# Performance work log

Hardware: AMD Instinct MI355X
Metric: run time of the kernel (lower is better)

The kernel has to match this reference:

```python
import jax, jax.numpy as jnp
import numpy as np

# Irrep layout of node_vec: 128x0e | 64x1e (64*3) | 32x2e (32*5)
MUL0, MUL1, MUL2 = 128, 64, 32
A = 32  # node_attr scalar channels (32x0e)
N = 8192


def setup_inputs() -> dict:
    key = jax.random.key(0)
    ks = jax.random.split(key, 12)
    f32 = jnp.float32
    return {
        "node_vec": jax.random.normal(ks[0], (N, MUL0 + 3 * MUL1 + 5 * MUL2), f32),
        "node_embedding": jax.random.normal(ks[1], (N, A), f32),
        # fctp_1: TP(input, attr) -> gated irreps (scalars + gates + vectors)
        "W1s": jax.random.normal(ks[2], (MUL0, A, MUL0), f32),          # 0e x 0e -> 0e
        "b1s": jnp.zeros((MUL0,), f32),
        "W1g": jax.random.normal(ks[3], (MUL0, A, MUL1 + MUL2), f32),   # 0e x 0e -> gate 0e
        "b1g": jnp.zeros((MUL1 + MUL2,), f32),
        "W1v1": jax.random.normal(ks[4], (MUL1, A, MUL1), f32),         # 1e x 0e -> 1e
        "W1v2": jax.random.normal(ks[5], (MUL2, A, MUL2), f32),         # 2e x 0e -> 2e
        # fctp_2: TP(mlp_mid, attr) -> 32x0e (only scalar path allowed by CG rules)
        "W2": jax.random.normal(ks[6], (MUL0, A, A), f32),
        "b2": jnp.zeros((A,), f32),
        # output network: LinearRS(32->32) + SiLU + LinearRS(32->1)
        "W3": jax.random.normal(ks[7], (A, A), f32),
        "b3": jnp.zeros((A,), f32),
        "W4": jax.random.normal(ks[8], (A, 1), f32),
        "b4": jnp.zeros((1,), f32),
    }


def reference(node_vec, node_embedding, W1s, b1s, W1g, b1g, W1v1, W1v2, W2, b2, W3, b3, W4, b4):
    n = node_vec.shape[0]
    attr = node_embedding
    # split features by irrep degree
    s = node_vec[:, :MUL0]                                         # [n,128]   0e
    v1 = node_vec[:, MUL0:MUL0 + 3 * MUL1].reshape(n, MUL1, 3)     # [n,64,3]  1e
    v2 = node_vec[:, MUL0 + 3 * MUL1:].reshape(n, MUL2, 5)         # [n,32,5]  2e

    inv = lambda u: 1.0 / np.sqrt(u * A).astype(np.float32)

    # ---- fctp_1: fully-connected TP with scalar attr (l x 0e -> l per-path mixing) ----
    s_mid = jnp.einsum('nu,nv,uvw->nw', s, attr, W1s) * inv(MUL0) + b1s
    g = jnp.einsum('nu,nv,uvw->nw', s, attr, W1g) * inv(MUL0) + b1g
    v1_mid = jnp.einsum('num,nv,uvw->nwm', v1, attr, W1v1) * inv(MUL1)
    v2_mid = jnp.einsum('num,nv,uvw->nwm', v2, attr, W1v2) * inv(MUL2)

    # ---- SwishGate: SiLU on scalars, sigmoid gates on vectors ----
    s_act = jax.nn.silu(s_mid)
    gate = jax.nn.sigmoid(g)
    v1_g = v1_mid * gate[:, :MUL1, None]
    v2_g = v2_mid * gate[:, MUL1:, None]
    # NOTE: v1_g/v2_g have no allowed CG path into the 0e output of fctp_2 (l x 0 -> 0
    # only for l=0), so they do not contribute — exactly as in the original module.
    del v1_g, v2_g

    # ---- fctp_2: mlp_mid x attr -> 32x0e (scalar path only) ----
    h = jnp.einsum('nu,nv,uvw->nw', s_act, attr, W2) * inv(MUL0) + b2

    # ---- output network: LinearRS + SiLU + LinearRS ----
    h = jax.nn.silu(h @ (W3 / np.sqrt(A).astype(np.float32)) + b3)
    pred_energy = h @ (W4 / np.sqrt(A).astype(np.float32)) + b4     # [n,1]
    return pred_energy
```

## Files before the change

kernel.cpp:

```cpp
#include <hip/hip_runtime.h>

typedef _Float16 f16;
typedef f16 f16x8 __attribute__((ext_vector_type(8)));
typedef f16 f16x4 __attribute__((ext_vector_type(4)));
typedef float f32x4 __attribute__((ext_vector_type(4)));

__global__ __launch_bounds__(256) void prep_kernel(
    const float* __restrict__ node_vec, const float* __restrict__ W1s,
    const float* __restrict__ W2, f16* __restrict__ s_bf,
    f16* __restrict__ W1G, f16* __restrict__ W2G)
{
    const int b = blockIdx.x, t = threadIdx.x;
    if (b < 512) {
        int j = b * 256 + t;
        int n = j >> 4, c8 = (j & 15) * 8;
        float4 a = *(const float4*)(node_vec + (size_t)n * 480 + c8);
        float4 c = *(const float4*)(node_vec + (size_t)n * 480 + c8 + 4);
        f16x8 o = { (f16)a.x, (f16)a.y, (f16)a.z, (f16)a.w,
                    (f16)c.x, (f16)c.y, (f16)c.z, (f16)c.w };
        *(f16x8*)(s_bf + (size_t)n * 128 + c8) = o;
    } else if (b < 1024) {
        int bb = b - 512;
        int cb = bb >> 2, u0 = (bb & 3) * 32;
        int v = t >> 3, u = u0 + (t & 7) * 4;
        f16x4 o = { (f16)W1s[(size_t)(u + 0) * 4096 + v * 128 + cb],
                    (f16)W1s[(size_t)(u + 1) * 4096 + v * 128 + cb],
                    (f16)W1s[(size_t)(u + 2) * 4096 + v * 128 + cb],
                    (f16)W1s[(size_t)(u + 3) * 4096 + v * 128 + cb] };
        *(f16x4*)(W1G + (size_t)(32 * cb + v) * 128 + u) = o;
    } else {
        int bb = b - 1024;
        int cb = bb >> 2, u0 = (bb & 3) * 32;
        int v = t >> 3, u = u0 + (t & 7) * 4;
        f16x4 o = { (f16)W2[(size_t)(u + 0) * 1024 + v * 32 + cb],
                    (f16)W2[(size_t)(u + 1) * 1024 + v * 32 + cb],
                    (f16)W2[(size_t)(u + 2) * 1024 + v * 32 + cb],
                    (f16)W2[(size_t)(u + 3) * 1024 + v * 32 + cb] };
        *(f16x4*)(W2G + (size_t)(32 * cb + v) * 128 + u) = o;
    }
}

template <int SILU>
__global__ __launch_bounds__(256, 2) void gemm_g(
    const f16* __restrict__ A, const f16* __restrict__ B,
    const float* __restrict__ attr, const float* __restrict__ bias,
    void* __restrict__ out)
{
    __shared__ __align__(16) unsigned char smem[69632];
    f16* A_lds = (f16*)smem;
    f16* B_lds = (f16*)smem + 128 * 136;

    const int t  = threadIdx.x;
    const int n0 = blockIdx.x * 128;
    const int c0 = blockIdx.y * 128;

    #pragma unroll
    for (int i = 0; i < 8; ++i) {
        int idx = t + 256 * i;
        int r = idx >> 4, c8 = (idx & 15) * 8;
        *(uint4*)(A_lds + r * 136 + c8) = *(const uint4*)(A + (size_t)(n0 + r) * 128 + c8);
        *(uint4*)(B_lds + r * 136 + c8) = *(const uint4*)(B + (size_t)(c0 + r) * 128 + c8);
    }
    __syncthreads();

    const int wv = t >> 6, l = t & 63, lr = l & 15, q = l >> 4;
    const int r0 = 32 * wv;

    f32x4 acc0[8], acc1[8];
    #pragma unroll
    for (int ct = 0; ct < 8; ++ct) { acc0[ct] = f32x4{0,0,0,0}; acc1[ct] = f32x4{0,0,0,0}; }

    #pragma unroll
    for (int ks = 0; ks < 4; ++ks) {
        f16x8 a0 = *(const f16x8*)(A_lds + (r0 + lr) * 136 + ks * 32 + q * 8);
        f16x8 a1 = *(const f16x8*)(A_lds + (r0 + 16 + lr) * 136 + ks * 32 + q * 8);
        #pragma unroll
        for (int ct = 0; ct < 8; ++ct) {
            f16x8 bf = *(const f16x8*)(B_lds + (16 * ct + lr) * 136 + ks * 32 + q * 8);
            acc0[ct] = __builtin_amdgcn_mfma_f32_16x16x32_f16(a0, bf, acc0[ct], 0, 0, 0);
            acc1[ct] = __builtin_amdgcn_mfma_f32_16x16x32_f16(a1, bf, acc1[ct], 0, 0, 0);
        }
    }

    float at[2][4][2];
    #pragma unroll
    for (int mt = 0; mt < 2; ++mt)
        #pragma unroll
        for (int reg = 0; reg < 4; ++reg) {
            int row = n0 + r0 + 16 * mt + q * 4 + reg;
            at[mt][reg][0] = attr[(size_t)row * 32 + lr];
            at[mt][reg][1] = attr[(size_t)row * 32 + 16 + lr];
        }

    #pragma unroll
    for (int mt = 0; mt < 2; ++mt)
        #pragma unroll
        for (int w = 0; w < 4; ++w) {
            f32x4 e0 = mt ? acc1[2 * w] : acc0[2 * w];
            f32x4 e1 = mt ? acc1[2 * w + 1] : acc0[2 * w + 1];
            float pv[4];
            #pragma unroll
            for (int reg = 0; reg < 4; ++reg)
                pv[reg] = e0[reg] * at[mt][reg][0] + e1[reg] * at[mt][reg][1];
            #pragma unroll
            for (int m = 1; m <= 8; m <<= 1) {
                #pragma unroll
                for (int reg = 0; reg < 4; ++reg)
                    pv[reg] += __shfl_xor(pv[reg], m);
            }
            if (lr == 0) {
                int wglob = (c0 >> 5) + w;
                float bv = bias[wglob];
                #pragma unroll
                for (int reg = 0; reg < 4; ++reg) {
                    int row = n0 + r0 + 16 * mt + q * 4 + reg;
                    float val = pv[reg] * 0.015625f + bv;
                    if (SILU) {
                        ((f16*)out)[(size_t)row * 128 + wglob] =
                            (f16)(val / (1.f + __expf(-val)));
                    } else {
                        ((float*)out)[(size_t)row * 32 + wglob] = val;
                    }
                }
            }
        }
}

__global__ __launch_bounds__(256) void head_kernel(
    const float* __restrict__ h, const float* __restrict__ W3,
    const float* __restrict__ b3, const float* __restrict__ W4,
    const float* __restrict__ b4, float* __restrict__ out)
{
    int tid = blockIdx.x * 256 + threadIdx.x;
    int n = tid >> 5, j = tid & 31;
    const float inv = 0.17677669529663687f;
    const float* hr = h + (size_t)n * 32;
    float acc = 0.f;
    #pragma unroll
    for (int i = 0; i < 32; ++i) acc += hr[i] * W3[i * 32 + j];
    float tv = acc * inv + b3[j];
    float g  = tv / (1.f + __expf(-tv));
    float p  = g * W4[j] * inv;
    #pragma unroll
    for (int m = 16; m >= 1; m >>= 1) p += __shfl_xor(p, m, 32);
    if (j == 0) out[n] = p + b4[0];
}

extern "C" void kernel_launch(void* const* d_in, const int* in_sizes, int n_in,
                              void* d_out, int out_size, void* d_ws, size_t ws_size,
                              hipStream_t stream)
{
    const float* node_vec = (const float*)d_in[0];
    const float* attr     = (const float*)d_in[1];
    const float* W1s      = (const float*)d_in[2];
    const float* b1s      = (const float*)d_in[3];
    const float* W2       = (const float*)d_in[8];
    const float* b2       = (const float*)d_in[9];
    const float* W3       = (const float*)d_in[10];
    const float* b3       = (const float*)d_in[11];
    const float* W4       = (const float*)d_in[12];
    const float* b4       = (const float*)d_in[13];
    float* out = (float*)d_out;

    char* ws = (char*)d_ws;
    f16*   s_bf  = (f16*)(ws);
    f16*   W1G   = (f16*)(ws + (2048u << 10));
    f16*   W2G   = (f16*)(ws + (3072u << 10));
    f16*   s_act = (f16*)(ws + (3328u << 10));
    float* h     = (float*)(ws + (5376u << 10));

    prep_kernel<<<1152, 256, 0, stream>>>(node_vec, W1s, W2, s_bf, W1G, W2G);
    gemm_g<1><<<dim3(64, 32), 256, 0, stream>>>(s_bf, W1G, attr, b1s, (void*)s_act);
    gemm_g<0><<<dim3(64, 8),  256, 0, stream>>>(s_act, W2G, attr, b2, (void*)h);
    head_kernel<<<1024, 256, 0, stream>>>(h, W3, b3, W4, b4, out);
}
```

Before: 131.6 us.

## Persist weight tile per block and loop over row subtiles with double-buffered A

```diff
diff --git a/kernel.cpp b/kernel.cpp
--- a/kernel.cpp
+++ b/kernel.cpp
@@ -40,90 +40,121 @@
     }
 }
 
-template <int SILU>
-__global__ __launch_bounds__(256, 2) void gemm_g(
+template <int NSUB, int SILU>
+__global__ __launch_bounds__(256, 1) void gemm_bs(
     const f16* __restrict__ A, const f16* __restrict__ B,
     const float* __restrict__ attr, const float* __restrict__ bias,
     void* __restrict__ out)
 {
-    __shared__ __align__(16) unsigned char smem[69632];
-    f16* A_lds = (f16*)smem;
-    f16* B_lds = (f16*)smem + 128 * 136;
+    __shared__ __align__(16) f16 B_lds[128 * 136];
+    __shared__ __align__(16) f16 A_lds[2][128 * 136];
 
     const int t  = threadIdx.x;
-    const int n0 = blockIdx.x * 128;
-    const int c0 = blockIdx.y * 128;
+    const int N0 = blockIdx.x * (NSUB * 128);
+    const int C0 = blockIdx.y * 128;
+    const int wv = t >> 6, l = t & 63, lr = l & 15, q = l >> 4;
+    const int R0 = 64 * (wv & 1);
+    const int CL = 64 * (wv >> 1);
 
     #pragma unroll
     for (int i = 0; i < 8; ++i) {
         int idx = t + 256 * i;
-        int r = idx >> 4, c8 = (idx & 15) * 8;
-        *(uint4*)(A_lds + r * 136 + c8) = *(const uint4*)(A + (size_t)(n0 + r) * 128 + c8);
-        *(uint4*)(B_lds + r * 136 + c8) = *(const uint4*)(B + (size_t)(c0 + r) * 128 + c8);
-    }
-    __syncthreads();
-
-    const int wv = t >> 6, l = t & 63, lr = l & 15, q = l >> 4;
-    const int r0 = 32 * wv;
-
-    f32x4 acc0[8], acc1[8];
-    #pragma unroll
-    for (int ct = 0; ct < 8; ++ct) { acc0[ct] = f32x4{0,0,0,0}; acc1[ct] = f32x4{0,0,0,0}; }
-
-    #pragma unroll
-    for (int ks = 0; ks < 4; ++ks) {
-        f16x8 a0 = *(const f16x8*)(A_lds + (r0 + lr) * 136 + ks * 32 + q * 8);
-        f16x8 a1 = *(const f16x8*)(A_lds + (r0 + 16 + lr) * 136 + ks * 32 + q * 8);
-        #pragma unroll
-        for (int ct = 0; ct < 8; ++ct) {
-            f16x8 bf = *(const f16x8*)(B_lds + (16 * ct + lr) * 136 + ks * 32 + q * 8);
-            acc0[ct] = __builtin_amdgcn_mfma_f32_16x16x32_f16(a0, bf, acc0[ct], 0, 0, 0);
-            acc1[ct] = __builtin_amdgcn_mfma_f32_16x16x32_f16(a1, bf, acc1[ct], 0, 0, 0);
-        }
-    }
-
-    float at[2][4][2];
-    #pragma unroll
-    for (int mt = 0; mt < 2; ++mt)
-        #pragma unroll
-        for (int reg = 0; reg < 4; ++reg) {
-            int row = n0 + r0 + 16 * mt + q * 4 + reg;
-            at[mt][reg][0] = attr[(size_t)row * 32 + lr];
-            at[mt][reg][1] = attr[(size_t)row * 32 + 16 + lr];
-        }
-
-    #pragma unroll
-    for (int mt = 0; mt < 2; ++mt)
-        #pragma unroll
-        for (int w = 0; w < 4; ++w) {
-            f32x4 e0 = mt ? acc1[2 * w] : acc0[2 * w];
-            f32x4 e1 = mt ? acc1[2 * w + 1] : acc0[2 * w + 1];
-            float pv[4];
-            #pragma unroll
-            for (int reg = 0; reg < 4; ++reg)
-                pv[reg] = e0[reg] * at[mt][reg][0] + e1[reg] * at[mt][reg][1];
-            #pragma unroll
-            for (int m = 1; m <= 8; m <<= 1) {
+        int r = idx >> 4, u0 = (idx & 15) * 8;
+        uint4 d = *(const uint4*)(B + (size_t)(C0 + r) * 128 + u0);
+        *(uint4*)(B_lds + r * 136 + u0) = d;
+    }
+
+    uint4 Ar[8];
+    #pragma unroll
+    for (int j = 0; j < 8; ++j) {
+        int idx = t + 256 * j;
+        int r = idx >> 4, u0 = (idx & 15) * 8;
+        Ar[j] = *(const uint4*)(A + (size_t)(N0 + r) * 128 + u0);
+    }
+
+    #pragma unroll
+    for (int i = 0; i < NSUB; ++i) {
+        const int buf = i & 1;
+
+        #pragma unroll
+        for (int j = 0; j < 8; ++j) {
+            int idx = t + 256 * j;
+            int r = idx >> 4, u0 = (idx & 15) * 8;
+            *(uint4*)(A_lds[buf] + r * 136 + u0) = Ar[j];
+        }
+        if (i + 1 < NSUB) {
+            #pragma unroll
+            for (int j = 0; j < 8; ++j) {
+                int idx = t + 256 * j;
+                int r = idx >> 4, u0 = (idx & 15) * 8;
+                Ar[j] = *(const uint4*)(A + (size_t)(N0 + (i + 1) * 128 + r) * 128 + u0);
+            }
+        }
+        __syncthreads();
+
+        f32x4 acc[4][4];
+        #pragma unroll
+        for (int mt = 0; mt < 4; ++mt)
+            #pragma unroll
+            for (int ct = 0; ct < 4; ++ct) acc[mt][ct] = f32x4{0, 0, 0, 0};
+
+        #pragma unroll
+        for (int ks = 0; ks < 4; ++ks) {
+            f16x8 af[4], bf[4];
+            #pragma unroll
+            for (int mt = 0; mt < 4; ++mt)
+                af[mt] = *(const f16x8*)(A_lds[buf] + (R0 + 16 * mt + lr) * 136 + ks * 32 + q * 8);
+            #pragma unroll
+            for (int ct = 0; ct < 4; ++ct)
+                bf[ct] = *(const f16x8*)(B_lds + (CL + 16 * ct + lr) * 136 + ks * 32 + q * 8);
+            #pragma unroll
+            for (int mt = 0; mt < 4; ++mt)
+                #pragma unroll
+                for (int ct = 0; ct < 4; ++ct)
+                    acc[mt][ct] = __builtin_amdgcn_mfma_f32_16x16x32_f16(
+                        af[mt], bf[ct], acc[mt][ct], 0, 0, 0);
+        }
+
+        #pragma unroll
+        for (int mt = 0; mt < 4; ++mt) {
+            float at0[4], at1[4];
+            #pragma unroll
+            for (int reg = 0; reg < 4; ++reg) {
+                int row = N0 + i * 128 + R0 + 16 * mt + q * 4 + reg;
+                at0[reg] = attr[(size_t)row * 32 + lr];
+                at1[reg] = attr[(size_t)row * 32 + 16 + lr];
+            }
+            #pragma unroll
+            for (int w = 0; w < 2; ++w) {
+                float pv[4];
                 #pragma unroll
                 for (int reg = 0; reg < 4; ++reg)
-                    pv[reg] += __shfl_xor(pv[reg], m);
-            }
-            if (lr == 0) {
-                int wglob = (c0 >> 5) + w;
-                float bv = bias[wglob];
+                    pv[reg] = acc[mt][2 * w][reg] * at0[reg]
+                            + acc[mt][2 * w + 1][reg] * at1[reg];
                 #pragma unroll
-                for (int reg = 0; reg < 4; ++reg) {
-                    int row = n0 + r0 + 16 * mt + q * 4 + reg;
-                    float val = pv[reg] * 0.015625f + bv;
-                    if (SILU) {
-                        ((f16*)out)[(size_t)row * 128 + wglob] =
-                            (f16)(val / (1.f + __expf(-val)));
-                    } else {
-                        ((float*)out)[(size_t)row * 32 + wglob] = val;
+                for (int m = 1; m <= 8; m <<= 1)
+                    #pragma unroll
+                    for (int reg = 0; reg < 4; ++reg)
+                        pv[reg] += __shfl_xor(pv[reg], m);
+                if (lr == 0) {
+                    int wg = blockIdx.y * 4 + (wv >> 1) * 2 + w;
+                    float bv = bias[wg];
+                    #pragma unroll
+                    for (int reg = 0; reg < 4; ++reg) {
+                        int row = N0 + i * 128 + R0 + 16 * mt + q * 4 + reg;
+                        float val = pv[reg] * 0.015625f + bv;
+                        if (SILU) {
+                            ((f16*)out)[(size_t)row * 128 + wg] =
+                                (f16)(val / (1.f + __expf(-val)));
+                        } else {
+                            ((float*)out)[(size_t)row * 32 + wg] = val;
+                        }
                     }
                 }
             }
         }
+        __syncthreads();
+    }
 }
 
 __global__ __launch_bounds__(256) void head_kernel(
@@ -170,7 +201,7 @@
     float* h     = (float*)(ws + (5376u << 10));
 
     prep_kernel<<<1152, 256, 0, stream>>>(node_vec, W1s, W2, s_bf, W1G, W2G);
-    gemm_g<1><<<dim3(64, 32), 256, 0, stream>>>(s_bf, W1G, attr, b1s, (void*)s_act);
-    gemm_g<0><<<dim3(64, 8),  256, 0, stream>>>(s_act, W2G, attr, b2, (void*)h);
+    gemm_bs<8, 1><<<dim3(8, 32), 256, 0, stream>>>(s_bf, W1G, attr, b1s, (void*)s_act);
+    gemm_bs<2, 0><<<dim3(32, 8), 256, 0, stream>>>(s_act, W2G, attr, b2, (void*)h);
     head_kernel<<<1024, 256, 0, stream>>>(h, W3, b3, W4, b4, out);
 }
```

Result: slower. 188.6 us (+43.3%).
